# Optimization experiments

Measured on AMD Instinct MI355X. Metric: run time of the kernel, lower is better.

Reference implementation:

```python
import jax, jax.numpy as jnp
import numpy as np

N = 50000       # nodes
E = 800000      # edges (before self-loops)
F = 128         # input features
H = 4           # heads
C = 64          # hidden per head
NC = 40         # classes
NEG_SLOPE = 0.2  # PyG GATConv default leaky relu slope


def _glorot(key, shape):
    fan = sum(shape[-2:]) if len(shape) >= 2 else shape[-1] * 2
    return jax.random.normal(key, shape, jnp.float32) * jnp.sqrt(2.0 / fan)


def gat_conv(x, W, a_src, a_dst, bias, src, dst, concat):
    """PyG-style GATConv (eval mode, self-loops already in src/dst).
    x:[N,Fin] W:[Fin,H*C] a_src,a_dst:[H,C] bias:[H*C] or [C]."""
    n = x.shape[0]
    h_, c_ = a_src.shape
    h = (x @ W).reshape(n, h_, c_)                      # [N,H,C]
    al_s = jnp.einsum('nhc,hc->nh', h, a_src)           # [N,H]
    al_d = jnp.einsum('nhc,hc->nh', h, a_dst)
    logits = jax.nn.leaky_relu(al_s[src] + al_d[dst], NEG_SLOPE)  # [E,H]
    # segment softmax over incoming edges of each dst node
    mx = jax.ops.segment_max(logits, dst, num_segments=n)
    mx = jnp.where(jnp.isfinite(mx), mx, 0.0)
    ex = jnp.exp(logits - mx[dst])
    den = jax.ops.segment_sum(ex, dst, num_segments=n)
    alpha = ex / (den[dst] + 1e-16)                     # [E,H]
    msg = h[src] * alpha[:, :, None]                    # [E,H,C]
    out = jax.ops.segment_sum(msg, dst, num_segments=n) # [N,H,C]
    if concat:
        return out.reshape(n, h_ * c_) + bias
    return out.mean(axis=1) + bias


def setup_inputs() -> dict:
    key = jax.random.key(0)
    ks = jax.random.split(key, 16)
    x = jax.random.normal(ks[0], (N, F), jnp.float32)
    edge_index = jax.random.randint(ks[1], (2, E), 0, N, jnp.int64)
    HC = H * C
    return {
        'x': x, 'edge_index': edge_index,
        'W1': _glorot(ks[2], (F, HC)),   'a1_src': _glorot(ks[3], (H, C)),
        'a1_dst': _glorot(ks[4], (H, C)), 'b1': jnp.zeros((HC,), jnp.float32),
        'W2': _glorot(ks[5], (HC, HC)),  'a2_src': _glorot(ks[6], (H, C)),
        'a2_dst': _glorot(ks[7], (H, C)), 'b2': jnp.zeros((HC,), jnp.float32),
        'W3': _glorot(ks[8], (HC, H * NC)), 'a3_src': _glorot(ks[9], (H, NC)),
        'a3_dst': _glorot(ks[10], (H, NC)), 'b3': jnp.zeros((NC,), jnp.float32),
    }


def reference(x, edge_index, W1, a1_src, a1_dst, b1, W2, a2_src, a2_dst, b2,
              W3, a3_src, a3_dst, b3):
    n = x.shape[0]
    loop = jnp.arange(n, dtype=edge_index.dtype)
    src = jnp.concatenate([edge_index[0], loop])
    dst = jnp.concatenate([edge_index[1], loop])
    x1 = jax.nn.elu(gat_conv(x, W1, a1_src, a1_dst, b1, src, dst, True))
    x2 = jax.nn.elu(gat_conv(x1, W2, a2_src, a2_dst, b2, src, dst, True) + x1)
    out = gat_conv(x2, W3, a3_src, a3_dst, b3, src, dst, False)  # [N,NC]
    return out
```

## Files before the change

### kernel.cpp

```cpp
#include <hip/hip_runtime.h>
#include <hip/hip_bf16.h>
#include <hip/hip_fp16.h>
#include <math.h>

#define NEG_SLOPE 0.2f

typedef _Float16 half8 __attribute__((ext_vector_type(8)));
typedef _Float16 half4 __attribute__((ext_vector_type(4)));
typedef float f32x4 __attribute__((ext_vector_type(4)));

__global__ void degree_kernel(const int* __restrict__ ei, int E, int n,
                              int* __restrict__ deg) {
    int e = blockIdx.x * 256 + threadIdx.x;
    int tot = E + n;
    if (e >= tot) return;
    int d = (e < E) ? ei[E + e] : (e - E);
    atomicAdd(&deg[d], 1);
}

__global__ __launch_bounds__(1024) void scan_block(const int* __restrict__ deg,
                                                   int* __restrict__ row_off,
                                                   int* __restrict__ bsums, int n) {
    __shared__ int tmp[1024];
    int t = threadIdx.x;
    int idx = blockIdx.x * 1024 + t;
    int v = (idx < n) ? deg[idx] : 0;
    tmp[t] = v;
    __syncthreads();
    #pragma unroll
    for (int off = 1; off < 1024; off <<= 1) {
        int x = (t >= off) ? tmp[t - off] : 0;
        __syncthreads();
        tmp[t] += x;
        __syncthreads();
    }
    if (idx < n) row_off[idx] = tmp[t] - v;
    if (t == 1023) bsums[blockIdx.x] = tmp[1023];
}

__global__ __launch_bounds__(64) void scan_sums(int* __restrict__ bsums, int nb,
                                                int* __restrict__ row_off, int n) {
    int lane = threadIdx.x;
    int carry = 0;
    for (int base = 0; base < nb; base += 64) {
        int i = base + lane;
        int o = (i < nb) ? bsums[i] : 0;
        int v = o;
        #pragma unroll
        for (int off = 1; off < 64; off <<= 1) {
            int x = __shfl_up(v, off, 64);
            if (lane >= off) v += x;
        }
        if (i < nb) bsums[i] = carry + v - o;
        int tot = __shfl(v, 63, 64);
        carry += tot;
    }
    if (lane == 0) row_off[n] = carry;
}

__global__ __launch_bounds__(1024) void scan_add(int* __restrict__ row_off,
                                                 const int* __restrict__ bsums,
                                                 int* __restrict__ cursor, int n) {
    int idx = blockIdx.x * 1024 + threadIdx.x;
    if (idx < n) {
        int v = row_off[idx] + bsums[blockIdx.x];
        row_off[idx] = v;
        cursor[idx] = v;
    }
}

__global__ void scatter_kernel(const int* __restrict__ ei, int E, int n,
                               int* __restrict__ cursor, int* __restrict__ csr_src) {
    int e = blockIdx.x * 256 + threadIdx.x;
    int tot = E + n;
    if (e >= tot) return;
    int s, d;
    if (e < E) { s = ei[e]; d = ei[E + e]; } else { s = d = e - E; }
    int pos = atomicAdd(&cursor[d], 1);
    csr_src[pos] = s;
}

__global__ void split_f32x4(const float* __restrict__ src, _Float16* __restrict__ hi,
                            _Float16* __restrict__ lo, int n4) {
    int i = blockIdx.x * 256 + threadIdx.x;
    if (i >= n4) return;
    float4 v = ((const float4*)src)[i];
    half4 h, l;
    h.x = (_Float16)v.x; l.x = (_Float16)(v.x - (float)h.x);
    h.y = (_Float16)v.y; l.y = (_Float16)(v.y - (float)h.y);
    h.z = (_Float16)v.z; l.z = (_Float16)(v.z - (float)h.z);
    h.w = (_Float16)v.w; l.w = (_Float16)(v.w - (float)h.w);
    ((half4*)hi)[i] = h;
    ((half4*)lo)[i] = l;
}

__global__ void wt_split(const float* __restrict__ W, _Float16* __restrict__ bhi,
                         _Float16* __restrict__ blo, int K, int N, int padN) {
    int idx = blockIdx.x * 256 + threadIdx.x;
    if (idx >= padN * K) return;
    int n = idx / K, k = idx % K;
    float v = (n < N) ? W[(size_t)k * N + n] : 0.f;
    _Float16 h = (_Float16)v;
    bhi[idx] = h;
    blo[idx] = (_Float16)(v - (float)h);
}

__global__ __launch_bounds__(256) void gemm_mfma(const _Float16* __restrict__ Ahi,
                                                 const _Float16* __restrict__ Alo,
                                                 const _Float16* __restrict__ Bthi,
                                                 const _Float16* __restrict__ Btlo,
                                                 float* __restrict__ C,
                                                 _Float16* __restrict__ Ch,
                                                 const float* __restrict__ a_src,
                                                 const float* __restrict__ a_dst,
                                                 float* __restrict__ als,
                                                 float* __restrict__ ald,
                                                 int M, int N, int K) {
    __shared__ _Float16 Ah[2][128 * 32];
    int t = threadIdx.x;
    int wave = t >> 6, lane = t & 63;
    int row0 = blockIdx.x * 128, col0 = blockIdx.y * 128;
    int wr = wave >> 1, wc = wave & 1;

    f32x4 acc[4][4];
    #pragma unroll
    for (int i = 0; i < 4; i++)
        #pragma unroll
        for (int j = 0; j < 4; j++)
            acc[i][j] = (f32x4)0.f;

    auto lds_off = [](int m, int g0) -> int {
        int P = m >> 1;
        int gp = ((m & 1) << 2) | g0;
        return P * 64 + ((gp ^ (P & 7)) << 3);
    };

    for (int k0 = 0; k0 < K; k0 += 32) {
        __syncthreads();
        #pragma unroll
        for (int i = 0; i < 2; i++) {
            int s = t + i * 256;
            int r = s >> 2, g0 = s & 3;
            int grow = row0 + r;
            half8 vh = {}, vl = {};
            if (grow < M) {
                vh = *(const half8*)(Ahi + (size_t)grow * K + k0 + g0 * 8);
                vl = *(const half8*)(Alo + (size_t)grow * K + k0 + g0 * 8);
            }
            int off = lds_off(r, g0);
            *(half8*)(&Ah[0][off]) = vh;
            *(half8*)(&Ah[1][off]) = vl;
        }
        __syncthreads();

        half8 bh[4], bl[4];
        #pragma unroll
        for (int nf = 0; nf < 4; nf++) {
            int n = col0 + wc * 64 + nf * 16 + (lane & 15);
            size_t bo = (size_t)n * K + k0 + (lane >> 4) * 8;
            bh[nf] = *(const half8*)(Bthi + bo);
            bl[nf] = *(const half8*)(Btlo + bo);
        }
        half8 ah[4], al[4];
        #pragma unroll
        for (int mf = 0; mf < 4; mf++) {
            int m = wr * 64 + mf * 16 + (lane & 15);
            int off = lds_off(m, lane >> 4);
            ah[mf] = *(half8*)(&Ah[0][off]);
            al[mf] = *(half8*)(&Ah[1][off]);
        }
        #pragma unroll
        for (int mf = 0; mf < 4; mf++)
            #pragma unroll
            for (int nf = 0; nf < 4; nf++) {
                acc[mf][nf] = __builtin_amdgcn_mfma_f32_16x16x32_f16(
                    ah[mf], bh[nf], acc[mf][nf], 0, 0, 0);
                acc[mf][nf] = __builtin_amdgcn_mfma_f32_16x16x32_f16(
                    ah[mf], bl[nf], acc[mf][nf], 0, 0, 0);
                acc[mf][nf] = __builtin_amdgcn_mfma_f32_16x16x32_f16(
                    al[mf], bh[nf], acc[mf][nf], 0, 0, 0);
            }
    }

    #pragma unroll
    for (int mf = 0; mf < 4; mf++)
        #pragma unroll
        for (int nf = 0; nf < 4; nf++) {
            int col = col0 + wc * 64 + nf * 16 + (lane & 15);
            if (col >= N) continue;
            #pragma unroll
            for (int q = 0; q < 4; q++) {
                int row = row0 + wr * 64 + mf * 16 + (lane >> 4) * 4 + q;
                if (row < M) {
                    float v = acc[mf][nf][q];
                    if (C) C[(size_t)row * N + col] = v;
                    Ch[(size_t)row * N + col] = (_Float16)v;
                }
            }
        }

    if (a_src) {
        int hblk = blockIdx.y * 2 + wc;
        float asv[4], adv[4];
        #pragma unroll
        for (int nf = 0; nf < 4; nf++) {
            int cih = nf * 16 + (lane & 15);
            asv[nf] = a_src[hblk * 64 + cih];
            adv[nf] = a_dst[hblk * 64 + cih];
        }
        #pragma unroll
        for (int mf = 0; mf < 4; mf++)
            #pragma unroll
            for (int q = 0; q < 4; q++) {
                float ss = 0.f, sd = 0.f;
                #pragma unroll
                for (int nf = 0; nf < 4; nf++) {
                    float v = acc[mf][nf][q];
                    ss = fmaf(v, asv[nf], ss);
                    sd = fmaf(v, adv[nf], sd);
                }
                #pragma unroll
                for (int off = 8; off >= 1; off >>= 1) {
                    ss += __shfl_xor(ss, off, 64);
                    sd += __shfl_xor(sd, off, 64);
                }
                int row = row0 + wr * 64 + mf * 16 + (lane >> 4) * 4 + q;
                if ((lane & 15) == 0 && row < M) {
                    als[row * 4 + hblk] = ss;
                    ald[row * 4 + hblk] = sd;
                }
            }
    }
}

template <int C>
__global__ __launch_bounds__(256) void coef_kernel(const float* __restrict__ h,
                                                   const float* __restrict__ a_src,
                                                   const float* __restrict__ a_dst,
                                                   float* __restrict__ als,
                                                   float* __restrict__ ald, int n) {
    int wave = threadIdx.x >> 6;
    int lane = threadIdx.x & 63;
    int node = blockIdx.x * 4 + wave;
    if (node >= n) return;
    const float* hr = h + (size_t)node * (4 * C);
    float ps[4], pd[4];
    #pragma unroll
    for (int hh = 0; hh < 4; hh++) {
        float hv = (lane < C) ? hr[hh * C + lane] : 0.f;
        float as_ = (lane < C) ? a_src[hh * C + lane] : 0.f;
        float ad_ = (lane < C) ? a_dst[hh * C + lane] : 0.f;
        ps[hh] = hv * as_;
        pd[hh] = hv * ad_;
    }
    #pragma unroll
    for (int off = 32; off >= 1; off >>= 1) {
        #pragma unroll
        for (int hh = 0; hh < 4; hh++) {
            ps[hh] += __shfl_xor(ps[hh], off, 64);
            pd[hh] += __shfl_xor(pd[hh], off, 64);
        }
    }
    if (lane == 0) {
        #pragma unroll
        for (int hh = 0; hh < 4; hh++) {
            als[node * 4 + hh] = ps[hh];
            ald[node * 4 + hh] = pd[hh];
        }
    }
}

template <int C, int MODE>
__global__ __launch_bounds__(256) void agg_kernel(const __half* __restrict__ hhp,
                                                  const float* __restrict__ als,
                                                  const float* __restrict__ ald,
                                                  const int* __restrict__ row_off,
                                                  const int* __restrict__ csr_src,
                                                  const float* __restrict__ bias,
                                                  const _Float16* __restrict__ rh,
                                                  const _Float16* __restrict__ rl,
                                                  float* __restrict__ outf,
                                                  _Float16* __restrict__ oh,
                                                  _Float16* __restrict__ ol, int n) {
    constexpr int HC = 4 * C;
    constexpr int LPN = HC / 8;
    constexpr int LPH = C / 8;
    const _Float16* hh = (const _Float16*)hhp;

    int t = threadIdx.x;
    int wave = t >> 6, lane = t & 63;
    int l = lane & 31;
    int node = (blockIdx.x * 4 + wave) * 2 + (lane >> 5);
    bool nact = node < n;
    bool lact = nact && (l < LPN);
    int g = (l < LPN) ? (l / LPH) : 0;

    int rs = 0, cnt = 0;
    if (lact) {
        rs = row_off[node];
        cnt = row_off[node + 1] - rs;
    }
    float aldg = lact ? ald[node * 4 + g] : 0.f;

    float acc[8] = {};
    float den = 0.f;

    if (cnt > 0) {
        int sA[8];
        float avA[8];
        #pragma unroll
        for (int q = 0; q < 8; q++) {
            int idx = q < cnt ? q : cnt - 1;
            sA[q] = csr_src[rs + idx];
        }
        #pragma unroll
        for (int q = 0; q < 8; q++) avA[q] = als[sA[q] * 4 + g];

        for (int base = 0; base < cnt; base += 8) {
            half8 hv[8];
            #pragma unroll
            for (int q = 0; q < 8; q++)
                hv[q] = *(const half8*)(hh + (size_t)sA[q] * HC + l * 8);

            int sB[8];
            float avB[8];
            if (base + 8 < cnt) {
                #pragma unroll
                for (int q = 0; q < 8; q++) {
                    int idx = base + 8 + q; if (idx >= cnt) idx = cnt - 1;
                    sB[q] = csr_src[rs + idx];
                }
                #pragma unroll
                for (int q = 0; q < 8; q++) avB[q] = als[sB[q] * 4 + g];
            }

            float ex[8];
            #pragma unroll
            for (int q = 0; q < 8; q++) {
                float lg = avA[q] + aldg;
                lg = (lg > 0.f) ? lg : NEG_SLOPE * lg;
                float e = __expf(lg);
                ex[q] = (base + q < cnt) ? e : 0.f;
                den += ex[q];
            }
            #pragma unroll
            for (int q = 0; q < 8; q++) {
                #pragma unroll
                for (int k = 0; k < 8; k++)
                    acc[k] = fmaf(ex[q], (float)hv[q][k], acc[k]);
            }
            #pragma unroll
            for (int q = 0; q < 8; q++) { sA[q] = sB[q]; avA[q] = avB[q]; }
        }
    }

    float inv = 1.f / (den + 1e-16f);
    float v[8];
    #pragma unroll
    for (int k = 0; k < 8; k++) v[k] = acc[k] * inv;

    if (MODE == 2) {
        float vs[8];
        #pragma unroll
        for (int k = 0; k < 8; k++) vs[k] = v[k];
        #pragma unroll
        for (int k2 = 1; k2 < 4; k2++) {
            #pragma unroll
            for (int k = 0; k < 8; k++)
                vs[k] += __shfl(v[k], lane + 5 * k2, 64);
        }
        if (nact && l < 5) {
            float b[8];
            *(float4*)&b[0] = *(const float4*)(bias + l * 8);
            *(float4*)&b[4] = *(const float4*)(bias + l * 8 + 4);
            float o[8];
            #pragma unroll
            for (int k = 0; k < 8; k++) o[k] = vs[k] * 0.25f + b[k];
            *(float4*)(outf + (size_t)node * C + l * 8)     = make_float4(o[0], o[1], o[2], o[3]);
            *(float4*)(outf + (size_t)node * C + l * 8 + 4) = make_float4(o[4], o[5], o[6], o[7]);
        }
    } else {
        if (lact) {
            float b[8];
            *(float4*)&b[0] = *(const float4*)(bias + l * 8);
            *(float4*)&b[4] = *(const float4*)(bias + l * 8 + 4);
            float o[8];
            #pragma unroll
            for (int k = 0; k < 8; k++) o[k] = v[k] + b[k];
            if (MODE == 1) {
                size_t ridx = (size_t)node * HC + l * 8;
                half8 r_h = *(const half8*)(rh + ridx);
                half8 r_l = *(const half8*)(rl + ridx);
                #pragma unroll
                for (int k = 0; k < 8; k++) o[k] += (float)r_h[k] + (float)r_l[k];
            }
            #pragma unroll
            for (int k = 0; k < 8; k++) o[k] = (o[k] > 0.f) ? o[k] : expm1f(o[k]);
            half8 hv8, lv8;
            #pragma unroll
            for (int k = 0; k < 8; k++) {
                hv8[k] = (_Float16)o[k];
                lv8[k] = (_Float16)(o[k] - (float)hv8[k]);
            }
            size_t oidx = (size_t)node * HC + l * 8;
            *(half8*)(oh + oidx) = hv8;
            *(half8*)(ol + oidx) = lv8;
        }
    }
}

extern "C" void kernel_launch(void* const* d_in, const int* in_sizes, int n_in,
                              void* d_out, int out_size, void* d_ws, size_t ws_size,
                              hipStream_t stream) {
    const float* x   = (const float*)d_in[0];
    const int*   ei  = (const int*)d_in[1];
    const float* W1  = (const float*)d_in[2];
    const float* a1s = (const float*)d_in[3];
    const float* a1d = (const float*)d_in[4];
    const float* b1  = (const float*)d_in[5];
    const float* W2  = (const float*)d_in[6];
    const float* a2s = (const float*)d_in[7];
    const float* a2d = (const float*)d_in[8];
    const float* b2  = (const float*)d_in[9];
    const float* W3  = (const float*)d_in[10];
    const float* a3s = (const float*)d_in[11];
    const float* a3d = (const float*)d_in[12];
    const float* b3  = (const float*)d_in[13];
    float* out = (float*)d_out;

    int N = in_sizes[0] / 128;
    int E = in_sizes[1] / 2;

    char* ws = (char*)d_ws;
    size_t off = 0;
    auto alloc = [&](size_t bytes) -> void* {
        void* p = ws + off;
        off += (bytes + 255) & ~(size_t)255;
        return p;
    };
    float*    hbuf  = (float*)alloc((size_t)N * 256 * 4);
    _Float16* hhalf = (_Float16*)alloc((size_t)N * 256 * 2);
    _Float16* pA_hi = (_Float16*)alloc((size_t)N * 256 * 2);
    _Float16* pA_lo = (_Float16*)alloc((size_t)N * 256 * 2);
    _Float16* pB_hi = (_Float16*)alloc((size_t)N * 256 * 2);
    _Float16* pB_lo = (_Float16*)alloc((size_t)N * 256 * 2);
    float*    als   = (float*)alloc((size_t)N * 4 * 4);
    float*    ald   = (float*)alloc((size_t)N * 4 * 4);
    _Float16* bt1h  = (_Float16*)alloc(256 * 128 * 2);
    _Float16* bt1l  = (_Float16*)alloc(256 * 128 * 2);
    _Float16* bt2h  = (_Float16*)alloc(256 * 256 * 2);
    _Float16* bt2l  = (_Float16*)alloc(256 * 256 * 2);
    _Float16* bt3h  = (_Float16*)alloc(256 * 256 * 2);
    _Float16* bt3l  = (_Float16*)alloc(256 * 256 * 2);
    int* deg     = (int*)alloc((size_t)N * 4);
    int* row_off = (int*)alloc((size_t)(N + 1) * 4);
    int* cursor  = (int*)alloc((size_t)N * 4);
    int* csr     = (int*)alloc((size_t)(E + N) * 4);
    int* bsums   = (int*)alloc(1024 * 4);

    int tot = E + N;
    int nb = (N + 1023) / 1024;
    hipMemsetAsync(deg, 0, (size_t)N * 4, stream);
    degree_kernel<<<(tot + 255) / 256, 256, 0, stream>>>(ei, E, N, deg);
    scan_block<<<nb, 1024, 0, stream>>>(deg, row_off, bsums, N);
    scan_sums<<<1, 64, 0, stream>>>(bsums, nb, row_off, N);
    scan_add<<<nb, 1024, 0, stream>>>(row_off, bsums, cursor, N);
    scatter_kernel<<<(tot + 255) / 256, 256, 0, stream>>>(ei, E, N, cursor, csr);

    {
        int n4 = N * 128 / 4;
        split_f32x4<<<(n4 + 255) / 256, 256, 0, stream>>>(x, pA_hi, pA_lo, n4);
        wt_split<<<(256 * 128 + 255) / 256, 256, 0, stream>>>(W1, bt1h, bt1l, 128, 256, 256);
        wt_split<<<(256 * 256 + 255) / 256, 256, 0, stream>>>(W2, bt2h, bt2l, 256, 256, 256);
        wt_split<<<(256 * 256 + 255) / 256, 256, 0, stream>>>(W3, bt3h, bt3l, 256, 160, 256);
    }

    int nodeBlocks4 = (N + 3) / 4;
    int nodeBlocks8 = (N + 7) / 8;
    dim3 blk(256);
    dim3 ggrid((N + 127) / 128, 2);

    gemm_mfma<<<ggrid, blk, 0, stream>>>(pA_hi, pA_lo, bt1h, bt1l, nullptr, hhalf,
                                         a1s, a1d, als, ald, N, 256, 128);
    agg_kernel<64, 0><<<nodeBlocks8, blk, 0, stream>>>((const __half*)hhalf, als, ald,
        row_off, csr, b1, nullptr, nullptr, nullptr, pB_hi, pB_lo, N);

    gemm_mfma<<<ggrid, blk, 0, stream>>>(pB_hi, pB_lo, bt2h, bt2l, nullptr, hhalf,
                                         a2s, a2d, als, ald, N, 256, 256);
    agg_kernel<64, 1><<<nodeBlocks8, blk, 0, stream>>>((const __half*)hhalf, als, ald,
        row_off, csr, b2, pB_hi, pB_lo, nullptr, pA_hi, pA_lo, N);

    gemm_mfma<<<ggrid, blk, 0, stream>>>(pA_hi, pA_lo, bt3h, bt3l, hbuf, hhalf,
                                         nullptr, nullptr, nullptr, nullptr, N, 160, 256);
    coef_kernel<40><<<nodeBlocks4, blk, 0, stream>>>(hbuf, a3s, a3d, als, ald, N);
    agg_kernel<40, 2><<<nodeBlocks8, blk, 0, stream>>>((const __half*)hhalf, als, ald,
        row_off, csr, b3, nullptr, nullptr, out, nullptr, nullptr, N);
}
```

Measured before the change: 492.7 us.

## Double-buffer GEMM LDS tiles, drop fp32 h output, persistent agg grid

The GEMM now double-buffers the A tile in LDS, prefetching the next K slice into registers while the MFMAs run on the current one, so each iteration needs one barrier instead of two. The fp32 copy of the layer-3 projection is no longer written; coef_kernel reads the fp16 buffer instead. This cuts store traffic but computes the layer-3 attention coefficients from fp16-rounded values. The aggregation kernels switch to a grid-stride loop over node pairs with the grid capped at 2048 blocks.

```diff
diff --git a/kernel.cpp b/kernel.cpp
--- a/kernel.cpp
+++ b/kernel.cpp
@@ -109,14 +109,13 @@
                                                  const _Float16* __restrict__ Alo,
                                                  const _Float16* __restrict__ Bthi,
                                                  const _Float16* __restrict__ Btlo,
-                                                 float* __restrict__ C,
                                                  _Float16* __restrict__ Ch,
                                                  const float* __restrict__ a_src,
                                                  const float* __restrict__ a_dst,
                                                  float* __restrict__ als,
                                                  float* __restrict__ ald,
                                                  int M, int N, int K) {
-    __shared__ _Float16 Ah[2][128 * 32];
+    __shared__ _Float16 Ah[2][2][128 * 32];
     int t = threadIdx.x;
     int wave = t >> 6, lane = t & 63;
     int row0 = blockIdx.x * 128, col0 = blockIdx.y * 128;
@@ -135,39 +134,61 @@
         return P * 64 + ((gp ^ (P & 7)) << 3);
     };
 
-    for (int k0 = 0; k0 < K; k0 += 32) {
-        __syncthreads();
-        #pragma unroll
-        for (int i = 0; i < 2; i++) {
-            int s = t + i * 256;
-            int r = s >> 2, g0 = s & 3;
-            int grow = row0 + r;
-            half8 vh = {}, vl = {};
-            if (grow < M) {
-                vh = *(const half8*)(Ahi + (size_t)grow * K + k0 + g0 * 8);
-                vl = *(const half8*)(Alo + (size_t)grow * K + k0 + g0 * 8);
-            }
-            int off = lds_off(r, g0);
-            *(half8*)(&Ah[0][off]) = vh;
-            *(half8*)(&Ah[1][off]) = vl;
-        }
-        __syncthreads();
-
+    int s0 = t, s1 = t + 256;
+    int r0 = s0 >> 2, g00 = s0 & 3;
+    int r1 = s1 >> 2, g01 = s1 & 3;
+    int off0 = lds_off(r0, g00), off1 = lds_off(r1, g01);
+    bool m0ok = (row0 + r0) < M, m1ok = (row0 + r1) < M;
+    const _Float16* a0h = Ahi + (size_t)(row0 + r0) * K + g00 * 8;
+    const _Float16* a0l = Alo + (size_t)(row0 + r0) * K + g00 * 8;
+    const _Float16* a1h = Ahi + (size_t)(row0 + r1) * K + g01 * 8;
+    const _Float16* a1l = Alo + (size_t)(row0 + r1) * K + g01 * 8;
+
+    half8 svh0, svl0, svh1, svl1;
+    auto stage_load = [&](int k0) {
+        svh0 = svl0 = svh1 = svl1 = (half8)(_Float16)0.f;
+        if (m0ok) { svh0 = *(const half8*)(a0h + k0); svl0 = *(const half8*)(a0l + k0); }
+        if (m1ok) { svh1 = *(const half8*)(a1h + k0); svl1 = *(const half8*)(a1l + k0); }
+    };
+    auto stage_write = [&](int buf) {
+        *(half8*)(&Ah[buf][0][off0]) = svh0;
+        *(half8*)(&Ah[buf][1][off0]) = svl0;
+        *(half8*)(&Ah[buf][0][off1]) = svh1;
+        *(half8*)(&Ah[buf][1][off1]) = svl1;
+    };
+
+    int nk = K >> 5;
+    stage_load(0);
+    stage_write(0);
+    __syncthreads();
+
+    const _Float16* bhp[4];
+    const _Float16* blp[4];
+    #pragma unroll
+    for (int nf = 0; nf < 4; nf++) {
+        int n = col0 + wc * 64 + nf * 16 + (lane & 15);
+        bhp[nf] = Bthi + (size_t)n * K + (lane >> 4) * 8;
+        blp[nf] = Btlo + (size_t)n * K + (lane >> 4) * 8;
+    }
+
+    for (int kt = 0; kt < nk; kt++) {
+        int cur = kt & 1;
+        if (kt + 1 < nk) stage_load((kt + 1) << 5);
+
+        int k0 = kt << 5;
         half8 bh[4], bl[4];
         #pragma unroll
         for (int nf = 0; nf < 4; nf++) {
-            int n = col0 + wc * 64 + nf * 16 + (lane & 15);
-            size_t bo = (size_t)n * K + k0 + (lane >> 4) * 8;
-            bh[nf] = *(const half8*)(Bthi + bo);
-            bl[nf] = *(const half8*)(Btlo + bo);
+            bh[nf] = *(const half8*)(bhp[nf] + k0);
+            bl[nf] = *(const half8*)(blp[nf] + k0);
         }
         half8 ah[4], al[4];
         #pragma unroll
         for (int mf = 0; mf < 4; mf++) {
             int m = wr * 64 + mf * 16 + (lane & 15);
             int off = lds_off(m, lane >> 4);
-            ah[mf] = *(half8*)(&Ah[0][off]);
-            al[mf] = *(half8*)(&Ah[1][off]);
+            ah[mf] = *(half8*)(&Ah[cur][0][off]);
+            al[mf] = *(half8*)(&Ah[cur][1][off]);
         }
         #pragma unroll
         for (int mf = 0; mf < 4; mf++)
@@ -180,6 +201,10 @@
                 acc[mf][nf] = __builtin_amdgcn_mfma_f32_16x16x32_f16(
                     al[mf], bh[nf], acc[mf][nf], 0, 0, 0);
             }
+        if (kt + 1 < nk) {
+            stage_write(cur ^ 1);
+            __syncthreads();
+        }
     }
 
     #pragma unroll
@@ -191,11 +216,8 @@
             #pragma unroll
             for (int q = 0; q < 4; q++) {
                 int row = row0 + wr * 64 + mf * 16 + (lane >> 4) * 4 + q;
-                if (row < M) {
-                    float v = acc[mf][nf][q];
-                    if (C) C[(size_t)row * N + col] = v;
-                    Ch[(size_t)row * N + col] = (_Float16)v;
-                }
+                if (row < M)
+                    Ch[(size_t)row * N + col] = (_Float16)acc[mf][nf][q];
             }
         }
 
@@ -234,7 +256,7 @@
 }
 
 template <int C>
-__global__ __launch_bounds__(256) void coef_kernel(const float* __restrict__ h,
+__global__ __launch_bounds__(256) void coef_kernel(const _Float16* __restrict__ h,
                                                    const float* __restrict__ a_src,
                                                    const float* __restrict__ a_dst,
                                                    float* __restrict__ als,
@@ -243,11 +265,11 @@
     int lane = threadIdx.x & 63;
     int node = blockIdx.x * 4 + wave;
     if (node >= n) return;
-    const float* hr = h + (size_t)node * (4 * C);
+    const _Float16* hr = h + (size_t)node * (4 * C);
     float ps[4], pd[4];
     #pragma unroll
     for (int hh = 0; hh < 4; hh++) {
-        float hv = (lane < C) ? hr[hh * C + lane] : 0.f;
+        float hv = (lane < C) ? (float)hr[hh * C + lane] : 0.f;
         float as_ = (lane < C) ? a_src[hh * C + lane] : 0.f;
         float ad_ = (lane < C) ? a_dst[hh * C + lane] : 0.f;
         ps[hh] = hv * as_;
@@ -290,121 +312,125 @@
     int t = threadIdx.x;
     int wave = t >> 6, lane = t & 63;
     int l = lane & 31;
-    int node = (blockIdx.x * 4 + wave) * 2 + (lane >> 5);
-    bool nact = node < n;
-    bool lact = nact && (l < LPN);
-    int g = (l < LPN) ? (l / LPH) : 0;
-
-    int rs = 0, cnt = 0;
-    if (lact) {
-        rs = row_off[node];
-        cnt = row_off[node + 1] - rs;
-    }
-    float aldg = lact ? ald[node * 4 + g] : 0.f;
-
-    float acc[8] = {};
-    float den = 0.f;
-
-    if (cnt > 0) {
-        int sA[8];
-        float avA[8];
-        #pragma unroll
-        for (int q = 0; q < 8; q++) {
-            int idx = q < cnt ? q : cnt - 1;
-            sA[q] = csr_src[rs + idx];
-        }
-        #pragma unroll
-        for (int q = 0; q < 8; q++) avA[q] = als[sA[q] * 4 + g];
-
-        for (int base = 0; base < cnt; base += 8) {
-            half8 hv[8];
-            #pragma unroll
-            for (int q = 0; q < 8; q++)
-                hv[q] = *(const half8*)(hh + (size_t)sA[q] * HC + l * 8);
-
-            int sB[8];
-            float avB[8];
-            if (base + 8 < cnt) {
+    int pairs = (n + 1) >> 1;
+
+    for (int p = blockIdx.x * 4 + wave; p < pairs; p += gridDim.x * 4) {
+        int node = p * 2 + (lane >> 5);
+        bool nact = node < n;
+        bool lact = nact && (l < LPN);
+        int g = (l < LPN) ? (l / LPH) : 0;
+
+        int rs = 0, cnt = 0;
+        if (lact) {
+            rs = row_off[node];
+            cnt = row_off[node + 1] - rs;
+        }
+        float aldg = lact ? ald[node * 4 + g] : 0.f;
+
+        float acc[8] = {};
+        float den = 0.f;
+
+        if (cnt > 0) {
+            int sA[8];
+            float avA[8];
+            #pragma unroll
+            for (int q = 0; q < 8; q++) {
+                int idx = q < cnt ? q : cnt - 1;
+                sA[q] = csr_src[rs + idx];
+            }
+            #pragma unroll
+            for (int q = 0; q < 8; q++) avA[q] = als[sA[q] * 4 + g];
+
+            for (int base = 0; base < cnt; base += 8) {
+                half8 hv[8];
+                #pragma unroll
+                for (int q = 0; q < 8; q++)
+                    hv[q] = *(const half8*)(hh + (size_t)sA[q] * HC + l * 8);
+
+                int sB[8];
+                float avB[8];
+                if (base + 8 < cnt) {
+                    #pragma unroll
+                    for (int q = 0; q < 8; q++) {
+                        int idx = base + 8 + q; if (idx >= cnt) idx = cnt - 1;
+                        sB[q] = csr_src[rs + idx];
+                    }
+                    #pragma unroll
+                    for (int q = 0; q < 8; q++) avB[q] = als[sB[q] * 4 + g];
+                }
+
+                float ex[8];
                 #pragma unroll
                 for (int q = 0; q < 8; q++) {
-                    int idx = base + 8 + q; if (idx >= cnt) idx = cnt - 1;
-                    sB[q] = csr_src[rs + idx];
-                }
-                #pragma unroll
-                for (int q = 0; q < 8; q++) avB[q] = als[sB[q] * 4 + g];
-            }
-
-            float ex[8];
-            #pragma unroll
-            for (int q = 0; q < 8; q++) {
-                float lg = avA[q] + aldg;
-                lg = (lg > 0.f) ? lg : NEG_SLOPE * lg;
-                float e = __expf(lg);
-                ex[q] = (base + q < cnt) ? e : 0.f;
-                den += ex[q];
-            }
-            #pragma unroll
-            for (int q = 0; q < 8; q++) {
+                    float lg = avA[q] + aldg;
+                    lg = (lg > 0.f) ? lg : NEG_SLOPE * lg;
+                    float e = __expf(lg);
+                    ex[q] = (base + q < cnt) ? e : 0.f;
+                    den += ex[q];
+                }
+                #pragma unroll
+                for (int q = 0; q < 8; q++) {
+                    #pragma unroll
+                    for (int k = 0; k < 8; k++)
+                        acc[k] = fmaf(ex[q], (float)hv[q][k], acc[k]);
+                }
+                #pragma unroll
+                for (int q = 0; q < 8; q++) { sA[q] = sB[q]; avA[q] = avB[q]; }
+            }
+        }
+
+        float inv = 1.f / (den + 1e-16f);
+        float v[8];
+        #pragma unroll
+        for (int k = 0; k < 8; k++) v[k] = acc[k] * inv;
+
+        if (MODE == 2) {
+            float vs[8];
+            #pragma unroll
+            for (int k = 0; k < 8; k++) vs[k] = v[k];
+            #pragma unroll
+            for (int k2 = 1; k2 < 4; k2++) {
                 #pragma unroll
                 for (int k = 0; k < 8; k++)
-                    acc[k] = fmaf(ex[q], (float)hv[q][k], acc[k]);
-            }
-            #pragma unroll
-            for (int q = 0; q < 8; q++) { sA[q] = sB[q]; avA[q] = avB[q]; }
-        }
-    }
-
-    float inv = 1.f / (den + 1e-16f);
-    float v[8];
-    #pragma unroll
-    for (int k = 0; k < 8; k++) v[k] = acc[k] * inv;
-
-    if (MODE == 2) {
-        float vs[8];
-        #pragma unroll
-        for (int k = 0; k < 8; k++) vs[k] = v[k];
-        #pragma unroll
-        for (int k2 = 1; k2 < 4; k2++) {
-            #pragma unroll
-            for (int k = 0; k < 8; k++)
-                vs[k] += __shfl(v[k], lane + 5 * k2, 64);
-        }
-        if (nact && l < 5) {
-            float b[8];
-            *(float4*)&b[0] = *(const float4*)(bias + l * 8);
-            *(float4*)&b[4] = *(const float4*)(bias + l * 8 + 4);
-            float o[8];
-            #pragma unroll
-            for (int k = 0; k < 8; k++) o[k] = vs[k] * 0.25f + b[k];
-            *(float4*)(outf + (size_t)node * C + l * 8)     = make_float4(o[0], o[1], o[2], o[3]);
-            *(float4*)(outf + (size_t)node * C + l * 8 + 4) = make_float4(o[4], o[5], o[6], o[7]);
-        }
-    } else {
-        if (lact) {
-            float b[8];
-            *(float4*)&b[0] = *(const float4*)(bias + l * 8);
-            *(float4*)&b[4] = *(const float4*)(bias + l * 8 + 4);
-            float o[8];
-            #pragma unroll
-            for (int k = 0; k < 8; k++) o[k] = v[k] + b[k];
-            if (MODE == 1) {
-                size_t ridx = (size_t)node * HC + l * 8;
-                half8 r_h = *(const half8*)(rh + ridx);
-                half8 r_l = *(const half8*)(rl + ridx);
-                #pragma unroll
-                for (int k = 0; k < 8; k++) o[k] += (float)r_h[k] + (float)r_l[k];
-            }
-            #pragma unroll
-            for (int k = 0; k < 8; k++) o[k] = (o[k] > 0.f) ? o[k] : expm1f(o[k]);
-            half8 hv8, lv8;
-            #pragma unroll
-            for (int k = 0; k < 8; k++) {
-                hv8[k] = (_Float16)o[k];
-                lv8[k] = (_Float16)(o[k] - (float)hv8[k]);
-            }
-            size_t oidx = (size_t)node * HC + l * 8;
-            *(half8*)(oh + oidx) = hv8;
-            *(half8*)(ol + oidx) = lv8;
+                    vs[k] += __shfl(v[k], lane + 5 * k2, 64);
+            }
+            if (nact && l < 5) {
+                float b[8];
+                *(float4*)&b[0] = *(const float4*)(bias + l * 8);
+                *(float4*)&b[4] = *(const float4*)(bias + l * 8 + 4);
+                float o[8];
+                #pragma unroll
+                for (int k = 0; k < 8; k++) o[k] = vs[k] * 0.25f + b[k];
+                *(float4*)(outf + (size_t)node * C + l * 8)     = make_float4(o[0], o[1], o[2], o[3]);
+                *(float4*)(outf + (size_t)node * C + l * 8 + 4) = make_float4(o[4], o[5], o[6], o[7]);
+            }
+        } else {
+            if (lact) {
+                float b[8];
+                *(float4*)&b[0] = *(const float4*)(bias + l * 8);
+                *(float4*)&b[4] = *(const float4*)(bias + l * 8 + 4);
+                float o[8];
+                #pragma unroll
+                for (int k = 0; k < 8; k++) o[k] = v[k] + b[k];
+                if (MODE == 1) {
+                    size_t ridx = (size_t)node * HC + l * 8;
+                    half8 r_h = *(const half8*)(rh + ridx);
+                    half8 r_l = *(const half8*)(rl + ridx);
+                    #pragma unroll
+                    for (int k = 0; k < 8; k++) o[k] += (float)r_h[k] + (float)r_l[k];
+                }
+                #pragma unroll
+                for (int k = 0; k < 8; k++) o[k] = (o[k] > 0.f) ? o[k] : expm1f(o[k]);
+                half8 hv8, lv8;
+                #pragma unroll
+                for (int k = 0; k < 8; k++) {
+                    hv8[k] = (_Float16)o[k];
+                    lv8[k] = (_Float16)(o[k] - (float)hv8[k]);
+                }
+                size_t oidx = (size_t)node * HC + l * 8;
+                *(half8*)(oh + oidx) = hv8;
+                *(half8*)(ol + oidx) = lv8;
+            }
         }
     }
 }
@@ -438,7 +464,6 @@
         off += (bytes + 255) & ~(size_t)255;
         return p;
     };
-    float*    hbuf  = (float*)alloc((size_t)N * 256 * 4);
     _Float16* hhalf = (_Float16*)alloc((size_t)N * 256 * 2);
     _Float16* pA_hi = (_Float16*)alloc((size_t)N * 256 * 2);
     _Float16* pA_lo = (_Float16*)alloc((size_t)N * 256 * 2);
@@ -476,23 +501,25 @@
     }
 
     int nodeBlocks4 = (N + 3) / 4;
-    int nodeBlocks8 = (N + 7) / 8;
+    int pairs = (N + 1) / 2;
+    int aggBlocks = (pairs + 3) / 4;
+    if (aggBlocks > 2048) aggBlocks = 2048;
     dim3 blk(256);
     dim3 ggrid((N + 127) / 128, 2);
 
-    gemm_mfma<<<ggrid, blk, 0, stream>>>(pA_hi, pA_lo, bt1h, bt1l, nullptr, hhalf,
+    gemm_mfma<<<ggrid, blk, 0, stream>>>(pA_hi, pA_lo, bt1h, bt1l, hhalf,
                                          a1s, a1d, als, ald, N, 256, 128);
-    agg_kernel<64, 0><<<nodeBlocks8, blk, 0, stream>>>((const __half*)hhalf, als, ald,
+    agg_kernel<64, 0><<<aggBlocks, blk, 0, stream>>>((const __half*)hhalf, als, ald,
         row_off, csr, b1, nullptr, nullptr, nullptr, pB_hi, pB_lo, N);
 
-    gemm_mfma<<<ggrid, blk, 0, stream>>>(pB_hi, pB_lo, bt2h, bt2l, nullptr, hhalf,
+    gemm_mfma<<<ggrid, blk, 0, stream>>>(pB_hi, pB_lo, bt2h, bt2l, hhalf,
                                          a2s, a2d, als, ald, N, 256, 256);
-    agg_kernel<64, 1><<<nodeBlocks8, blk, 0, stream>>>((const __half*)hhalf, als, ald,
+    agg_kernel<64, 1><<<aggBlocks, blk, 0, stream>>>((const __half*)hhalf, als, ald,
         row_off, csr, b2, pB_hi, pB_lo, nullptr, pA_hi, pA_lo, N);
 
-    gemm_mfma<<<ggrid, blk, 0, stream>>>(pA_hi, pA_lo, bt3h, bt3l, hbuf, hhalf,
+    gemm_mfma<<<ggrid, blk, 0, stream>>>(pA_hi, pA_lo, bt3h, bt3l, hhalf,
                                          nullptr, nullptr, nullptr, nullptr, N, 160, 256);
-    coef_kernel<40><<<nodeBlocks4, blk, 0, stream>>>(hbuf, a3s, a3d, als, ald, N);
-    agg_kernel<40, 2><<<nodeBlocks8, blk, 0, stream>>>((const __half*)hhalf, als, ald,
+    coef_kernel<40><<<nodeBlocks4, blk, 0, stream>>>(hhalf, a3s, a3d, als, ald, N);
+    agg_kernel<40, 2><<<aggBlocks, blk, 0, stream>>>((const __half*)hhalf, als, ald,
         row_off, csr, b3, nullptr, nullptr, out, nullptr, nullptr, N);
 }
```

After: 488.7 us. About the same (-0.8%).
